# Performance work log

Measured on AMD Instinct MI355X. Metric: run time of the kernel, lower is better.

Reference implementation:

```python
import jax, jax.numpy as jnp
import numpy as np

NUM_GROUPS = 32
EPS = 1e-6


def group_norm(x, gamma, beta):
    # x: (b, c, h, w) -> normalize within 32 groups over (c/g, h, w)
    b, c, h, w = x.shape
    g = NUM_GROUPS
    xg = x.reshape(b, g, c // g, h, w)
    mean = xg.mean(axis=(2, 3, 4), keepdims=True)
    var = xg.var(axis=(2, 3, 4), keepdims=True)
    xg = (xg - mean) * jax.lax.rsqrt(var + EPS)
    xn = xg.reshape(b, c, h, w)
    return xn * gamma[None, :, None, None] + beta[None, :, None, None]


def setup_inputs() -> dict:
    key = jax.random.key(0)
    ks = jax.random.split(key, 4)
    b, c, h, w = 4, 512, 64, 64
    x = jax.random.normal(ks[0], (b, c, h, w), dtype=jnp.float32)
    gamma = jnp.ones((c,), dtype=jnp.float32)
    beta = jnp.zeros((c,), dtype=jnp.float32)
    w_qkv = jax.random.normal(ks[1], (3 * c, c), dtype=jnp.float32) * (1.0 / np.sqrt(c))
    b_qkv = jnp.zeros((3 * c,), dtype=jnp.float32)
    # NOTE: original init zeroes proj weight; use small random weights so the
    # attention path contributes to output/gradients in the baseline.
    w_proj = jax.random.normal(ks[2], (c, c), dtype=jnp.float32) * 0.02
    b_proj = jnp.zeros((c,), dtype=jnp.float32)
    return {"x": x, "gamma": gamma, "beta": beta, "w_qkv": w_qkv,
            "b_qkv": b_qkv, "w_proj": w_proj, "b_proj": b_proj}


def reference(x, gamma, beta, w_qkv, b_qkv, w_proj, b_proj):
    b, c, h, w = x.shape
    scale = c ** (-0.25)
    identity = x
    xn = group_norm(x, gamma, beta)
    # 1x1 conv == channel matmul: (b,c,h,w) x (3c,c) -> (b,3c,h,w)
    qkv = jnp.einsum('bchw,oc->bohw', xn, w_qkv) + b_qkv[None, :, None, None]
    qkv = qkv.reshape(b, 3 * c, h * w)
    q, k, v = jnp.split(qkv, 3, axis=1)          # each (b, c, N)
    attn = jnp.einsum('bci,bcj->bij', q * scale, k * scale)  # (b, N, N)
    attn = jax.nn.softmax(attn, axis=-1)
    out = jnp.einsum('bij,bcj->bci', attn, v)    # (b, c, N)
    out = out.reshape(b, c, h, w)
    out = jnp.einsum('bchw,oc->bohw', out, w_proj) + b_proj[None, :, None, None]
    return out + identity
```

## Files before the change

kernel.cpp:

```cpp
#include <hip/hip_runtime.h>
#include <hip/hip_fp8.h>
#include <stdint.h>

typedef unsigned short u16;
typedef unsigned char u8;
typedef __bf16 bf16x8 __attribute__((ext_vector_type(8)));
typedef float f32x4 __attribute__((ext_vector_type(4)));

__device__ __forceinline__ u16 f2bf(float f) {
  union { float f; unsigned u; } v; v.f = f;
  return (u16)((v.u + 0x7FFFu + ((v.u >> 16) & 1u)) >> 16);
}
__device__ __forceinline__ u8 f2f8(float f) {
  __hip_fp8_e4m3 h(f);
  return (u8)h.__x;
}

__device__ __forceinline__ void gld_lds16(const void* g, void* l) {
  uint32_t lo = (uint32_t)(uintptr_t)l;
  lo = __builtin_amdgcn_readfirstlane(lo);
  auto* lp = (__attribute__((address_space(3))) uint32_t*)(uintptr_t)lo;
  auto* gp = (const __attribute__((address_space(1))) uint32_t*)(uintptr_t)g;
  __builtin_amdgcn_global_load_lds(gp, lp, 16, 0, 0);
}

__device__ __forceinline__ void bar() {
  __builtin_amdgcn_sched_barrier(0);
  __builtin_amdgcn_s_barrier();
  __builtin_amdgcn_sched_barrier(0);
}

__global__ __launch_bounds__(256) void cvt_weights(
    const float* __restrict__ wq, const float* __restrict__ wp,
    u16* __restrict__ oq, u16* __restrict__ op) {
  int i = blockIdx.x * 256 + threadIdx.x;
  if (i < 1536 * 512) oq[i] = f2bf(wq[i]);
  if (i < 512 * 512)  op[i] = f2bf(wp[i]);
}

__global__ __launch_bounds__(256) void gn_stats(const float* __restrict__ x,
                                                float* __restrict__ stats) {
  int bg = blockIdx.x;
  const float* p = x + (size_t)bg * 65536;
  float s = 0.f, sq = 0.f;
  for (int i = threadIdx.x * 4; i < 65536; i += 1024) {
    float4 v = *(const float4*)(p + i);
    s += v.x + v.y + v.z + v.w;
    sq += v.x * v.x + v.y * v.y + v.z * v.z + v.w * v.w;
  }
  int lane = threadIdx.x & 63, w = threadIdx.x >> 6;
  for (int off = 32; off; off >>= 1) {
    s += __shfl_down(s, off);
    sq += __shfl_down(sq, off);
  }
  __shared__ float ls[4], lq[4];
  if (lane == 0) { ls[w] = s; lq[w] = sq; }
  __syncthreads();
  if (threadIdx.x == 0) {
    float S = ls[0] + ls[1] + ls[2] + ls[3];
    float Q = lq[0] + lq[1] + lq[2] + lq[3];
    float mean = S * (1.f / 65536.f);
    float var = Q * (1.f / 65536.f) - mean * mean;
    stats[bg * 2] = mean;
    stats[bg * 2 + 1] = rsqrtf(var + 1e-6f);
  }
}

__global__ __launch_bounds__(256) void gn_norm_t(const float* __restrict__ x,
    const float* __restrict__ stats, const float* __restrict__ gamma,
    const float* __restrict__ beta, u16* __restrict__ xnT) {
  __shared__ u16 tile[64][72];
  int b = blockIdx.z;
  int c0 = blockIdx.y * 64, n0 = blockIdx.x * 64;
  int t = threadIdx.x;
  int cl = t >> 2, ng = (t & 3) * 16;
  int c = c0 + cl;
  float mean = stats[(b * 32 + (c >> 4)) * 2];
  float rstd = stats[(b * 32 + (c >> 4)) * 2 + 1];
  float a = gamma[c] * rstd;
  float b2 = beta[c] - mean * a;
  const float* src = x + ((size_t)b * 512 + c) * 4096 + n0 + ng;
  u16 e[16];
  #pragma unroll
  for (int q = 0; q < 4; ++q) {
    float4 v = *(const float4*)(src + q * 4);
    e[q * 4 + 0] = f2bf(v.x * a + b2);
    e[q * 4 + 1] = f2bf(v.y * a + b2);
    e[q * 4 + 2] = f2bf(v.z * a + b2);
    e[q * 4 + 3] = f2bf(v.w * a + b2);
  }
  #pragma unroll
  for (int j = 0; j < 16; ++j) tile[ng + j][cl] = e[j];
  __syncthreads();
  int nl = t >> 2, cg = (t & 3) * 16;
  uint4 w0 = *(const uint4*)&tile[nl][cg];
  uint4 w1 = *(const uint4*)&tile[nl][cg + 8];
  u16* dst = xnT + ((size_t)b * 4096 + n0 + nl) * 512 + c0 + cg;
  *(uint4*)dst = w0;
  *(uint4*)(dst + 8) = w1;
}

template<int EPI>
__global__ __launch_bounds__(256) void gemm_nt(
    const u16* __restrict__ A, const u16* __restrict__ B,
    int lda, int ldb, int K,
    const float* __restrict__ bias, const float* __restrict__ resid,
    float scale, float* __restrict__ outF, void* __restrict__ outBv, int ldo,
    size_t azs, size_t bzs, size_t ozs) {
  __shared__ __align__(16) u16 smem[16384];
  const size_t z = blockIdx.z;
  A += z * azs; B += z * bzs;
  const int t = threadIdx.x;
  const int wave = t >> 6, lane = t & 63;
  const int wm = wave >> 1, wn = wave & 1;
  const int quad = lane >> 4, li = lane & 15;
  const int m0 = blockIdx.y * 128, n0 = blockIdx.x * 128;

  const int srow = lane >> 2;
  const int scol = (lane & 3) * 8;
  const u16* gA[2];
  const u16* gB[2];
  int ldsOff[2];
  #pragma unroll
  for (int r = 0; r < 2; ++r) {
    int rb = wave + 4 * r;
    gA[r] = A + (size_t)(m0 + rb * 16 + srow) * lda + scol;
    gB[r] = B + (size_t)(n0 + rb * 16 + srow) * ldb + scol;
    ldsOff[r] = rb * 512;
  }

  f32x4 zero = {0.f, 0.f, 0.f, 0.f};
  f32x4 acc[4][4];
  #pragma unroll
  for (int i = 0; i < 4; ++i)
    #pragma unroll
    for (int j = 0; j < 4; ++j) acc[i][j] = zero;

  #pragma unroll
  for (int r = 0; r < 2; ++r) {
    gld_lds16(gA[r], &smem[ldsOff[r]]);
    gld_lds16(gB[r], &smem[8192 + ldsOff[r]]);
  }
  __syncthreads();

  for (int kt = 0; kt < K; kt += 32) {
    const int s = (kt >> 5) & 1;
    if (kt + 32 < K) {
      const int ns = s ^ 1;
      #pragma unroll
      for (int r = 0; r < 2; ++r) {
        gld_lds16(gA[r] + kt + 32, &smem[ns * 4096 + ldsOff[r]]);
        gld_lds16(gB[r] + kt + 32, &smem[8192 + ns * 4096 + ldsOff[r]]);
      }
    }
    bf16x8 af[4], bf[4];
    #pragma unroll
    for (int i = 0; i < 4; ++i) {
      af[i] = *(const bf16x8*)&smem[s * 4096 +
               (wm * 64 + i * 16 + li) * 32 + quad * 8];
      bf[i] = *(const bf16x8*)&smem[8192 + s * 4096 +
               (wn * 64 + i * 16 + li) * 32 + quad * 8];
    }
    #pragma unroll
    for (int i = 0; i < 4; ++i)
      #pragma unroll
      for (int j = 0; j < 4; ++j)
        acc[i][j] = __builtin_amdgcn_mfma_f32_16x16x32_bf16(
            af[i], bf[j], acc[i][j], 0, 0, 0);
    __syncthreads();
  }

  if (EPI == 3) {
    outF += z * ozs; resid += z * ozs;
    #pragma unroll
    for (int i = 0; i < 4; ++i)
      #pragma unroll
      for (int j = 0; j < 4; ++j) {
        int mB = m0 + wm * 64 + i * 16 + quad * 4;
        int n = n0 + wn * 64 + j * 16 + li;
        #pragma unroll
        for (int r = 0; r < 4; ++r) {
          int m = mB + r;
          float v = acc[i][j][r] + bias[m] + resid[(size_t)m * ldo + n];
          outF[(size_t)m * ldo + n] = v;
        }
      }
    return;
  }

  u8* out8 = (u8*)outBv + z * ozs;
  u8* bnc = (u8*)smem;
  #pragma unroll
  for (int i = 0; i < 4; ++i) {
    int lm = wm * 64 + i * 16 + quad * 4;
    #pragma unroll
    for (int j = 0; j < 4; ++j) {
      int ln = wn * 64 + j * 16 + li;
      #pragma unroll
      for (int r = 0; r < 4; ++r) {
        float v = acc[i][j][r];
        u8 o;
        if (EPI == 4) o = f2f8((v + bias[n0 + ln]) * scale);
        else          o = f2f8(v + bias[m0 + lm + r]);
        bnc[(lm + r) * 144 + ln] = o;
      }
    }
  }
  __syncthreads();
  {
    int row = t >> 1, half = t & 1;
    const u8* src = &bnc[row * 144 + half * 64];
    u8* dst = out8 + (size_t)(m0 + row) * ldo + n0 + half * 64;
    #pragma unroll
    for (int cc = 0; cc < 4; ++cc)
      *(uint4*)(dst + cc * 16) = *(const uint4*)(src + cc * 16);
  }
}

template<int EPI, int SWZ>
__global__ __launch_bounds__(256) void gemm_nt8(
    const u8* __restrict__ A, const u8* __restrict__ B,
    int lda, int ldb, int K,
    const float* __restrict__ rsum, float* __restrict__ outF,
    void* __restrict__ outBv, int ldo,
    size_t azs, size_t bzs, size_t ozs) {
  __shared__ __align__(16) u8 smem[49152];
  const size_t z = blockIdx.z;
  A += z * azs; B += z * bzs;
  int bx = blockIdx.x, by = blockIdx.y;
  if (SWZ) {
    int lin = by * 32 + bx;
    int tt = lin >> 8, w = lin & 255;
    by = (tt >> 1) * 16 + (w >> 4);
    bx = (tt & 1) * 16 + (w & 15);
  }
  const int t = threadIdx.x;
  const int wave = t >> 6, lane = t & 63;
  const int wm = wave >> 1, wn = wave & 1;
  const int quad = lane >> 4, li = lane & 15;
  const int m0 = by * 128, n0 = bx * 128;

  const int us = lane ^ ((lane >> 3) & 7);
  const int srow = (us >> 1) & 31;
  const int shalf = us & 1;
  const u8* gA = A + (size_t)(m0 + wave * 32 + srow) * lda + shalf * 16;
  const u8* gB = B + (size_t)(n0 + wave * 32 + srow) * ldb + shalf * 16;
  const int ldsOff = wave * 1024;

  const int h = quad >> 1, qlo = (quad & 1) * 8;
  int aoff[4], boff[4];
  #pragma unroll
  for (int i = 0; i < 4; ++i) {
    int r5 = (i & 1) * 16 + li;
    int p = (2 * r5 + h) ^ ((r5 >> 2) & 7);
    aoff[i] = (wm * 2 + (i >> 1)) * 1024 + p * 16 + qlo;
    boff[i] = (wn * 2 + (i >> 1)) * 1024 + p * 16 + qlo;
  }

  f32x4 zero = {0.f, 0.f, 0.f, 0.f};
  f32x4 acc[4][4];
  #pragma unroll
  for (int i = 0; i < 4; ++i)
    #pragma unroll
    for (int j = 0; j < 4; ++j) acc[i][j] = zero;

  #pragma unroll
  for (int p = 0; p < 2; ++p) {
    gld_lds16(gA + p * 64,      &smem[p * 8192 + ldsOff]);
    gld_lds16(gA + p * 64 + 32, &smem[p * 8192 + 4096 + ldsOff]);
    gld_lds16(gB + p * 64,      &smem[24576 + p * 8192 + ldsOff]);
    gld_lds16(gB + p * 64 + 32, &smem[24576 + p * 8192 + 4096 + ldsOff]);
  }
  __builtin_amdgcn_sched_barrier(0);
  asm volatile("s_waitcnt vmcnt(4)");
  bar();

  int s = 0;
  for (int kt = 0; kt < K; kt += 64) {
    if (kt + 128 < K) {
      const int ns = (s == 0) ? 2 : s - 1;
      gld_lds16(gA + kt + 128,      &smem[ns * 8192 + ldsOff]);
      gld_lds16(gA + kt + 128 + 32, &smem[ns * 8192 + 4096 + ldsOff]);
      gld_lds16(gB + kt + 128,      &smem[24576 + ns * 8192 + ldsOff]);
      gld_lds16(gB + kt + 128 + 32, &smem[24576 + ns * 8192 + 4096 + ldsOff]);
    }
    const int sb = s * 8192;
    long af[4][2], bf[4][2];
    #pragma unroll
    for (int i = 0; i < 4; ++i) {
      #pragma unroll
      for (int g = 0; g < 2; ++g) {
        af[i][g] = *(const long*)&smem[sb + g * 4096 + aoff[i]];
        bf[i][g] = *(const long*)&smem[24576 + sb + g * 4096 + boff[i]];
      }
    }
    #pragma unroll
    for (int i = 0; i < 4; ++i)
      #pragma unroll
      for (int j = 0; j < 4; ++j) {
        acc[i][j] = __builtin_amdgcn_mfma_f32_16x16x32_fp8_fp8(
            af[i][0], bf[j][0], acc[i][j], 0, 0, 0);
        acc[i][j] = __builtin_amdgcn_mfma_f32_16x16x32_fp8_fp8(
            af[i][1], bf[j][1], acc[i][j], 0, 0, 0);
      }
    if (kt + 64 < K) {
      __builtin_amdgcn_sched_barrier(0);
      if (kt + 128 < K) asm volatile("s_waitcnt vmcnt(4)");
      else              asm volatile("s_waitcnt vmcnt(0)");
      bar();
    }
    s = (s == 2) ? 0 : s + 1;
  }
  __syncthreads();

  if (EPI == 7) {
    float* rsF = outF + z * 4096;
    u8* outE = (u8*)outBv + z * ozs;
    #pragma unroll
    for (int i = 0; i < 4; ++i) {
      int lm = wm * 64 + i * 16 + quad * 4;
      float rs[4] = {0.f, 0.f, 0.f, 0.f};
      #pragma unroll
      for (int j = 0; j < 4; ++j) {
        int ln = wn * 64 + j * 16 + li;
        #pragma unroll
        for (int r = 0; r < 4; ++r) {
          float e = fminf(__expf(acc[i][j][r]), 448.f);
          smem[(lm + r) * 144 + ln] = f2f8(e);
          rs[r] += e;
        }
      }
      #pragma unroll
      for (int r = 0; r < 4; ++r) {
        rs[r] += __shfl_xor(rs[r], 1);
        rs[r] += __shfl_xor(rs[r], 2);
        rs[r] += __shfl_xor(rs[r], 4);
        rs[r] += __shfl_xor(rs[r], 8);
      }
      if (li == 0) {
        #pragma unroll
        for (int r = 0; r < 4; ++r) atomicAdd(&rsF[m0 + lm + r], rs[r]);
      }
    }
    __syncthreads();
    int row = t >> 1, half = t & 1;
    const u8* src = &smem[row * 144 + half * 64];
    u8* dst = outE + (size_t)(m0 + row) * ldo + n0 + half * 64;
    #pragma unroll
    for (int cc = 0; cc < 4; ++cc)
      *(uint4*)(dst + cc * 16) = *(const uint4*)(src + cc * 16);
  } else {
    const float* rsF = rsum + z * 4096;
    u16* outp = (u16*)outBv + z * ozs;
    u16* b16 = (u16*)smem;
    #pragma unroll
    for (int i = 0; i < 4; ++i) {
      int lm = wm * 64 + i * 16 + quad * 4;
      float rinv[4];
      #pragma unroll
      for (int r = 0; r < 4; ++r)
        rinv[r] = __builtin_amdgcn_rcpf(rsF[m0 + lm + r]);
      #pragma unroll
      for (int j = 0; j < 4; ++j) {
        int ln = wn * 64 + j * 16 + li;
        #pragma unroll
        for (int r = 0; r < 4; ++r)
          b16[(lm + r) * 136 + ln] = f2bf(acc[i][j][r] * rinv[r]);
      }
    }
    __syncthreads();
    int row = t >> 1, half = t & 1;
    const u16* src = &b16[row * 136 + half * 64];
    u16* dst = outp + (size_t)(m0 + row) * ldo + n0 + half * 64;
    #pragma unroll
    for (int cc = 0; cc < 8; ++cc)
      *(uint4*)(dst + cc * 8) = *(const uint4*)(src + cc * 8);
  }
}

extern "C" void kernel_launch(void* const* d_in, const int* in_sizes, int n_in,
                              void* d_out, int out_size, void* d_ws, size_t ws_size,
                              hipStream_t stream) {
  (void)in_sizes; (void)n_in; (void)out_size; (void)ws_size;
  const float* x      = (const float*)d_in[0];
  const float* gamma  = (const float*)d_in[1];
  const float* beta   = (const float*)d_in[2];
  const float* w_qkv  = (const float*)d_in[3];
  const float* b_qkv  = (const float*)d_in[4];
  const float* w_proj = (const float*)d_in[5];
  const float* b_proj = (const float*)d_in[6];
  float* out = (float*)d_out;

  const int C = 512, N = 4096;
  const size_t NC = (size_t)N * C;
  const float scale = 0.21022410381342863f;

  char* ws = (char*)d_ws;
  size_t off = 0;
  auto alloc = [&](size_t bytes) -> char* {
    char* p = ws + off; off += (bytes + 255) & ~(size_t)255; return p;
  };
  u16*   wq_bf  = (u16*)alloc((size_t)1536 * 512 * 2);
  u16*   wp_bf  = (u16*)alloc((size_t)512 * 512 * 2);
  float* stats  = (float*)alloc(128 * 2 * 4);
  float* rowsum = (float*)alloc((size_t)4 * N * 4);
  u16*   xnT    = (u16*)alloc((size_t)4 * NC * 2);
  u8*    qkT    = (u8*)alloc((size_t)4 * N * 1024);
  u8*    vbf    = (u8*)alloc((size_t)4 * 512 * 4096);
  u16*   ao     = (u16*)alloc((size_t)4 * NC * 2);
  u8*    E      = (u8*)alloc((size_t)4 * N * N);

  cvt_weights<<<3072, 256, 0, stream>>>(w_qkv, w_proj, wq_bf, wp_bf);
  gn_stats<<<128, 256, 0, stream>>>(x, stats);
  gn_norm_t<<<dim3(64, 8, 4), 256, 0, stream>>>(x, stats, gamma, beta, xnT);
  hipMemsetAsync(rowsum, 0, (size_t)4 * N * 4, stream);

  gemm_nt<4><<<dim3(8, 32, 4), 256, 0, stream>>>(
      xnT, wq_bf, 512, 512, 512, b_qkv, nullptr, scale,
      nullptr, qkT, 1024, NC, 0, (size_t)N * 1024);
  gemm_nt<5><<<dim3(32, 4, 4), 256, 0, stream>>>(
      wq_bf + (size_t)1024 * 512, xnT, 512, 512, 512, b_qkv + 1024, nullptr,
      0.f, nullptr, vbf, 4096, 0, NC, (size_t)512 * 4096);
  gemm_nt8<7, 1><<<dim3(32, 32, 4), 256, 0, stream>>>(
      qkT, qkT + 512, 1024, 1024, 512, nullptr, rowsum,
      E, 4096, (size_t)N * 1024, (size_t)N * 1024, (size_t)N * N);
  gemm_nt8<6, 0><<<dim3(4, 32, 4), 256, 0, stream>>>(
      E, vbf, 4096, 4096, 4096, rowsum, nullptr,
      ao, 512, (size_t)N * N, (size_t)512 * 4096, NC);
  gemm_nt<3><<<dim3(32, 4, 4), 256, 0, stream>>>(
      wp_bf, ao, 512, 512, 512, b_proj, x, 0.f,
      out, nullptr, 4096, 0, NC, NC);
}
```

Baseline: 367.0 us.

## Add dedicated 256x128-tile fp8 QK^T kernel with fused exp and rowsum

Replaces the generic 128x128 fp8 GEMM used for the QK^T/exp stage with a specialized kernel that computes 256x128 tiles, each wave owning 64 rows by 128 columns. Every loaded B fragment is reused across more MFMAs, which cuts LDS and global traffic per output element. The epilogue keeps the exp, fp8 conversion and atomic rowsum, and each thread now writes a full 128-byte row. The cost is a larger accumulator (128 floats per thread) and 72KB of shared memory per block, which lowers occupancy.

```diff
diff --git a/kernel.cpp b/kernel.cpp
--- a/kernel.cpp
+++ b/kernel.cpp
@@ -313,43 +313,7 @@
   }
   __syncthreads();
 
-  if (EPI == 7) {
-    float* rsF = outF + z * 4096;
-    u8* outE = (u8*)outBv + z * ozs;
-    #pragma unroll
-    for (int i = 0; i < 4; ++i) {
-      int lm = wm * 64 + i * 16 + quad * 4;
-      float rs[4] = {0.f, 0.f, 0.f, 0.f};
-      #pragma unroll
-      for (int j = 0; j < 4; ++j) {
-        int ln = wn * 64 + j * 16 + li;
-        #pragma unroll
-        for (int r = 0; r < 4; ++r) {
-          float e = fminf(__expf(acc[i][j][r]), 448.f);
-          smem[(lm + r) * 144 + ln] = f2f8(e);
-          rs[r] += e;
-        }
-      }
-      #pragma unroll
-      for (int r = 0; r < 4; ++r) {
-        rs[r] += __shfl_xor(rs[r], 1);
-        rs[r] += __shfl_xor(rs[r], 2);
-        rs[r] += __shfl_xor(rs[r], 4);
-        rs[r] += __shfl_xor(rs[r], 8);
-      }
-      if (li == 0) {
-        #pragma unroll
-        for (int r = 0; r < 4; ++r) atomicAdd(&rsF[m0 + lm + r], rs[r]);
-      }
-    }
-    __syncthreads();
-    int row = t >> 1, half = t & 1;
-    const u8* src = &smem[row * 144 + half * 64];
-    u8* dst = outE + (size_t)(m0 + row) * ldo + n0 + half * 64;
-    #pragma unroll
-    for (int cc = 0; cc < 4; ++cc)
-      *(uint4*)(dst + cc * 16) = *(const uint4*)(src + cc * 16);
-  } else {
+  {
     const float* rsF = rsum + z * 4096;
     u16* outp = (u16*)outBv + z * ozs;
     u16* b16 = (u16*)smem;
@@ -375,6 +339,136 @@
     #pragma unroll
     for (int cc = 0; cc < 8; ++cc)
       *(uint4*)(dst + cc * 8) = *(const uint4*)(src + cc * 8);
+  }
+}
+
+__global__ __launch_bounds__(256) void qk256(
+    const u8* __restrict__ A, const u8* __restrict__ B,
+    float* __restrict__ rowsum, u8* __restrict__ outE) {
+  __shared__ __align__(16) u8 smem[73728];
+  const int lda = 1024, K = 512;
+  const size_t z = blockIdx.z;
+  A += (size_t)z * 4096 * 1024;
+  B += (size_t)z * 4096 * 1024;
+  float* rsF = rowsum + (size_t)z * 4096;
+  u8* outp = outE + (size_t)z * 4096 * 4096;
+
+  const int t = threadIdx.x;
+  const int w = t >> 6, lane = t & 63;
+  const int quad = lane >> 4, li = lane & 15;
+  const int m0 = blockIdx.y * 256, n0 = blockIdx.x * 128;
+
+  const int us = lane ^ ((lane >> 3) & 7);
+  const int srow = (us >> 1) & 31;
+  const int shalf = us & 1;
+  const u8* gA0 = A + (size_t)(m0 + w * 64 + srow) * lda + shalf * 16;
+  const u8* gA1 = gA0 + (size_t)32 * lda;
+  const u8* gB  = B + (size_t)(n0 + w * 32 + srow) * lda + shalf * 16;
+
+  const int h = quad >> 1, qlo = (quad & 1) * 8;
+  int aoff[4], boff[8];
+  #pragma unroll
+  for (int i = 0; i < 4; ++i) {
+    int r5 = (i & 1) * 16 + li;
+    int p = (2 * r5 + h) ^ ((r5 >> 2) & 7);
+    aoff[i] = (2 * w + (i >> 1)) * 1024 + p * 16 + qlo;
+  }
+  #pragma unroll
+  for (int j = 0; j < 8; ++j) {
+    int r5 = (j & 1) * 16 + li;
+    int p = (2 * r5 + h) ^ ((r5 >> 2) & 7);
+    boff[j] = (j >> 1) * 1024 + p * 16 + qlo;
+  }
+
+  f32x4 zero = {0.f, 0.f, 0.f, 0.f};
+  f32x4 acc[4][8];
+  #pragma unroll
+  for (int i = 0; i < 4; ++i)
+    #pragma unroll
+    for (int j = 0; j < 8; ++j) acc[i][j] = zero;
+
+  auto STAGE = [&](int kt, int st) {
+    int sA = st * 16384, sB = 49152 + st * 8192;
+    #pragma unroll
+    for (int g = 0; g < 2; ++g) {
+      gld_lds16(gA0 + kt + g * 32, &smem[sA + g * 8192 + (2 * w) * 1024]);
+      gld_lds16(gA1 + kt + g * 32, &smem[sA + g * 8192 + (2 * w + 1) * 1024]);
+      gld_lds16(gB  + kt + g * 32, &smem[sB + g * 4096 + w * 1024]);
+    }
+  };
+
+  STAGE(0, 0);
+  STAGE(64, 1);
+  __builtin_amdgcn_sched_barrier(0);
+  asm volatile("s_waitcnt vmcnt(6)");
+  bar();
+
+  int s = 0;
+  for (int kt = 0; kt < K; kt += 64) {
+    if (kt + 128 < K) STAGE(kt + 128, (s == 0) ? 2 : s - 1);
+    const int sA = s * 16384, sB = 49152 + s * 8192;
+    long af[4][2];
+    #pragma unroll
+    for (int i = 0; i < 4; ++i)
+      #pragma unroll
+      for (int g = 0; g < 2; ++g)
+        af[i][g] = *(const long*)&smem[sA + g * 8192 + aoff[i]];
+    #pragma unroll
+    for (int j = 0; j < 8; ++j) {
+      long b0 = *(const long*)&smem[sB + boff[j]];
+      long b1 = *(const long*)&smem[sB + 4096 + boff[j]];
+      #pragma unroll
+      for (int i = 0; i < 4; ++i) {
+        acc[i][j] = __builtin_amdgcn_mfma_f32_16x16x32_fp8_fp8(
+            af[i][0], b0, acc[i][j], 0, 0, 0);
+        acc[i][j] = __builtin_amdgcn_mfma_f32_16x16x32_fp8_fp8(
+            af[i][1], b1, acc[i][j], 0, 0, 0);
+      }
+    }
+    if (kt + 64 < K) {
+      __builtin_amdgcn_sched_barrier(0);
+      if (kt + 128 < K) asm volatile("s_waitcnt vmcnt(6)");
+      else              asm volatile("s_waitcnt vmcnt(0)");
+      bar();
+    }
+    s = (s == 2) ? 0 : s + 1;
+  }
+  __syncthreads();
+
+  #pragma unroll
+  for (int i = 0; i < 4; ++i) {
+    int lm = w * 64 + i * 16 + quad * 4;
+    float rs[4] = {0.f, 0.f, 0.f, 0.f};
+    #pragma unroll
+    for (int j = 0; j < 8; ++j) {
+      int ln = j * 16 + li;
+      #pragma unroll
+      for (int r = 0; r < 4; ++r) {
+        float e = fminf(__expf(acc[i][j][r]), 448.f);
+        smem[(lm + r) * 144 + ln] = f2f8(e);
+        rs[r] += e;
+      }
+    }
+    #pragma unroll
+    for (int r = 0; r < 4; ++r) {
+      rs[r] += __shfl_xor(rs[r], 1);
+      rs[r] += __shfl_xor(rs[r], 2);
+      rs[r] += __shfl_xor(rs[r], 4);
+      rs[r] += __shfl_xor(rs[r], 8);
+    }
+    if (li == 0) {
+      #pragma unroll
+      for (int r = 0; r < 4; ++r) atomicAdd(&rsF[m0 + lm + r], rs[r]);
+    }
+  }
+  __syncthreads();
+  {
+    int row = t;
+    const u8* src = &smem[row * 144];
+    u8* dst = outp + (size_t)(m0 + row) * 4096 + n0;
+    #pragma unroll
+    for (int cc = 0; cc < 8; ++cc)
+      *(uint4*)(dst + cc * 16) = *(const uint4*)(src + cc * 16);
   }
 }
 
@@ -421,9 +515,7 @@
   gemm_nt<5><<<dim3(32, 4, 4), 256, 0, stream>>>(
       wq_bf + (size_t)1024 * 512, xnT, 512, 512, 512, b_qkv + 1024, nullptr,
       0.f, nullptr, vbf, 4096, 0, NC, (size_t)512 * 4096);
-  gemm_nt8<7, 1><<<dim3(32, 32, 4), 256, 0, stream>>>(
-      qkT, qkT + 512, 1024, 1024, 512, nullptr, rowsum,
-      E, 4096, (size_t)N * 1024, (size_t)N * 1024, (size_t)N * N);
+  qk256<<<dim3(32, 16, 4), 256, 0, stream>>>(qkT, qkT + 512, rowsum, E);
   gemm_nt8<6, 0><<<dim3(4, 32, 4), 256, 0, stream>>>(
       E, vbf, 4096, 4096, 4096, rowsum, nullptr,
       ao, 512, (size_t)N * N, (size_t)512 * 4096, NC);
```

Measured after the change: 393.1 us. 7.1% more time.
